# Kernel tuning notes

Measured on AMD Instinct MI355X. Metric: run time of the kernel, lower is better.

The kernel has to match this reference:

```python
import jax, jax.numpy as jnp
import numpy as np

N_NODES = 50000
N_EDGES = 800000
IN_DIM = 256
HID = 256
NUM_LAYERS = 2


def _sage(xin, src, dst, inv_deg, W_l, b_l, W_r):
    # PyG SAGEConv (mean aggr): lin_l(mean of src features scattered to dst) + lin_r(x)
    agg = jax.ops.segment_sum(xin[src], dst, num_segments=xin.shape[0]) * inv_deg
    return agg @ W_l + b_l + xin @ W_r


def _mgdsgu(x, src, dst, inv_deg, h, Wx_l, bx_l, Wx_r, Wh_l, bh_l, Wh_r, Wb1, bb1, Wb2, bb2):
    # hid->hid conv order: 0=sage_hidden, 1=sage_single_h, 2=sage_update_h, 3=sage_candidate_h
    # in ->hid conv order: 0=sage_single_x, 1=sage_update_x, 2=sage_candidate_x
    h_N = _sage(h, src, dst, inv_deg, Wh_l[0], bh_l[0], Wh_r[0])
    # predict_missing_info: r = zeros so r_v = beta; gamma is computed in the
    # original but multiplied by zero -> no effect (omitted).
    beta = jnp.tanh(h @ Wb1 + bb1 + h_N @ Wb2 + bb2)
    m = h + beta - h_N
    h_N = h_N + m  # == h + beta, kept as written for clarity
    r = jax.nn.sigmoid(_sage(x, src, dst, inv_deg, Wx_l[0], bx_l[0], Wx_r[0])
                       + _sage(h_N, src, dst, inv_deg, Wh_l[1], bh_l[1], Wh_r[1]))
    z = jax.nn.sigmoid(_sage(x, src, dst, inv_deg, Wx_l[1], bx_l[1], Wx_r[1])
                       + _sage(h_N, src, dst, inv_deg, Wh_l[2], bh_l[2], Wh_r[2]))
    h_tilde = jnp.tanh(_sage(x, src, dst, inv_deg, Wx_l[2], bx_l[2], Wx_r[2])
                       + _sage(r * h_N, src, dst, inv_deg, Wh_l[3], bh_l[3], Wh_r[3]))
    return (1.0 - z) * h_N + z * h_tilde


def setup_inputs() -> dict:
    key = jax.random.key(0)
    ks = jax.random.split(key, 12)
    sx = 1.0 / np.sqrt(IN_DIM)
    sh = 1.0 / np.sqrt(HID)
    inp = {
        "x": jax.random.normal(ks[0], (N_NODES, IN_DIM), dtype=jnp.float32),
        "edge_index": jax.random.randint(ks[1], (2, N_EDGES), 0, N_NODES, dtype=jnp.int64),
        "Wx_l": jax.random.normal(ks[2], (3, IN_DIM, HID), dtype=jnp.float32) * sx,
        "bx_l": jnp.zeros((3, HID), dtype=jnp.float32),
        "Wx_r": jax.random.normal(ks[3], (3, IN_DIM, HID), dtype=jnp.float32) * sx,
        "Wh_l": jax.random.normal(ks[4], (4, HID, HID), dtype=jnp.float32) * sh,
        "bh_l": jnp.zeros((4, HID), dtype=jnp.float32),
        "Wh_r": jax.random.normal(ks[5], (4, HID, HID), dtype=jnp.float32) * sh,
        "Wb1": jax.random.normal(ks[6], (HID, HID), dtype=jnp.float32) * sh,
        "bb1": jnp.zeros((HID,), dtype=jnp.float32),
        "Wb2": jax.random.normal(ks[7], (HID, HID), dtype=jnp.float32) * sh,
        "bb2": jnp.zeros((HID,), dtype=jnp.float32),
        "We1": jax.random.normal(ks[8], (2 * HID, HID), dtype=jnp.float32) * (1.0 / np.sqrt(2 * HID)),
        "be1": jnp.zeros((HID,), dtype=jnp.float32),
        "We2": jax.random.normal(ks[9], (HID, 1), dtype=jnp.float32) * sh,
        "be2": jnp.zeros((1,), dtype=jnp.float32),
    }
    return inp


def reference(x, edge_index, Wx_l, bx_l, Wx_r, Wh_l, bh_l, Wh_r,
              Wb1, bb1, Wb2, bb2, We1, be1, We2, be2):
    src, dst = edge_index[0], edge_index[1]
    deg = jax.ops.segment_sum(jnp.ones((src.shape[0],), dtype=x.dtype), dst,
                              num_segments=x.shape[0])
    inv_deg = (1.0 / jnp.maximum(deg, 1.0))[:, None]  # [N, 1]

    h = jnp.zeros((x.shape[0], HID), dtype=x.dtype)
    for _ in range(NUM_LAYERS):
        h = _mgdsgu(x, src, dst, inv_deg, h, Wx_l, bx_l, Wx_r,
                    Wh_l, bh_l, Wh_r, Wb1, bb1, Wb2, bb2)

    # edge embeddings: concat(src emb, dst emb) -> MLP -> sigmoid
    edge_emb = jnp.concatenate([h[src], h[dst]], axis=1)  # [E, 2H]
    hidden = jax.nn.relu(edge_emb @ We1 + be1)
    preds = jax.nn.sigmoid(hidden @ We2 + be2)  # [E, 1]
    return (preds, h)
```

## Files before the change

kernel.cpp:

```cpp
#include <hip/hip_runtime.h>
#include <math.h>

#define HID 256
#define LROW 40

typedef __bf16 bf16x8 __attribute__((ext_vector_type(8)));
typedef float  f32x4  __attribute__((ext_vector_type(4)));
typedef unsigned short us8 __attribute__((ext_vector_type(8)));

__device__ __forceinline__ float sigmoidf_(float x){ return 1.0f/(1.0f + __expf(-x)); }
__device__ __forceinline__ unsigned short f2b(float f){
  __bf16 b = (__bf16)f; return __builtin_bit_cast(unsigned short, b);
}
__device__ __forceinline__ float b2f(unsigned short u){
  return (float)__builtin_bit_cast(__bf16, u);
}

__device__ __forceinline__ int edge_src(const int* ei, int e, int is64){
  return is64 ? ei[2*e] : ei[e];
}
__device__ __forceinline__ int edge_dst(const int* ei, int e, int E, int is64){
  return is64 ? ei[2*(E+e)] : ei[E+e];
}

__global__ void detect_kernel(const int* __restrict__ ei, int* __restrict__ flag){
  __shared__ int any;
  if (threadIdx.x == 0) any = 0;
  __syncthreads();
  if (ei[2*threadIdx.x + 1] != 0) atomicOr(&any, 1);
  __syncthreads();
  if (threadIdx.x == 0) *flag = any ? 0 : 1;
}

__global__ void count_kernel(const int* __restrict__ ei, const int* __restrict__ flag,
                             int* __restrict__ deg_i, int E){
  int e = blockIdx.x*blockDim.x + threadIdx.x;
  if (e >= E) return;
  int is64 = *flag;
  atomicAdd(&deg_i[edge_dst(ei,e,E,is64)], 1);
}

__global__ __launch_bounds__(1024) void scan_kernel(const int* __restrict__ deg_i,
  int* __restrict__ row_ptr, float* __restrict__ inv_deg, int N)
{
  __shared__ int wsum[16];
  __shared__ int carry_s;
  int tid = threadIdx.x, lane = tid & 63, wid = tid >> 6;
  if (tid == 0) carry_s = 0;
  __syncthreads();
  for (int base = 0; base < N; base += 1024){
    int i = base + tid;
    int v = (i < N) ? deg_i[i] : 0;
    int s = v;
    #pragma unroll
    for (int off = 1; off < 64; off <<= 1){
      int t = __shfl_up(s, off, 64);
      if (lane >= off) s += t;
    }
    if (lane == 63) wsum[wid] = s;
    __syncthreads();
    if (tid == 0){
      int run = 0;
      for (int w2 = 0; w2 < 16; ++w2){ int t = wsum[w2]; wsum[w2] = run; run += t; }
    }
    __syncthreads();
    int excl = carry_s + wsum[wid] + s - v;
    if (i < N){
      row_ptr[i] = excl;
      inv_deg[i] = 1.0f / fmaxf((float)v, 1.0f);
    }
    __syncthreads();
    if (tid == 1023) carry_s = excl + v;
    __syncthreads();
  }
  if (threadIdx.x == 0) row_ptr[N] = carry_s;
}

__global__ void fill_kernel(const int* __restrict__ ei, const int* __restrict__ flag,
                            const int* __restrict__ row_ptr, int* __restrict__ cursor,
                            int* __restrict__ col_src, int E){
  int e = blockIdx.x*blockDim.x + threadIdx.x;
  if (e >= E) return;
  int is64 = *flag;
  int d = edge_dst(ei,e,E,is64);
  int pos = atomicAdd(&cursor[d], 1);
  col_src[row_ptr[d] + pos] = edge_src(ei,e,is64);
}

__global__ __launch_bounds__(256) void conv_kernel(const float* __restrict__ in,
                                                   unsigned short* __restrict__ out, int n4){
  int i = blockIdx.x*256 + threadIdx.x;
  if (i >= n4) return;
  float4 v = *(const float4*)&in[(size_t)i*4];
  ushort4 o; o.x=f2b(v.x); o.y=f2b(v.y); o.z=f2b(v.z); o.w=f2b(v.w);
  *(ushort4*)&out[(size_t)i*4] = o;
}

__global__ __launch_bounds__(256) void wconv_kernel(
  const float* __restrict__ Wx_l, const float* __restrict__ Wx_r,
  const float* __restrict__ Wh_l, const float* __restrict__ Wh_r,
  const float* __restrict__ Wb1,  const float* __restrict__ Wb2,
  const float* __restrict__ We1,  unsigned short* __restrict__ Wt)
{
  int widx = blockIdx.x;
  int n = blockIdx.y;
  int k = threadIdx.x;
  const float* src;
  if      (widx < 3)  src = Wx_l + widx*65536;
  else if (widx < 6)  src = Wx_r + (widx-3)*65536;
  else if (widx < 10) src = Wh_l + (widx-6)*65536;
  else if (widx < 14) src = Wh_r + (widx-10)*65536;
  else if (widx == 14) src = Wb1;
  else if (widx == 15) src = Wb2;
  else                src = We1 + (widx-16)*65536;
  Wt[(size_t)widx*65536 + n*256 + k] = f2b(src[k*256 + n]);
}

__global__ __launch_bounds__(256) void comp_kernel(
  const float* __restrict__ A, const float* __restrict__ B,
  const float* __restrict__ add, unsigned short* __restrict__ dst)
{
  __shared__ float col[256];
  int n = blockIdx.x, k = threadIdx.x;
  col[k] = B[k*256 + n];
  __syncthreads();
  float s = add ? add[k*256 + n] : 0.f;
  #pragma unroll 8
  for (int j = 0; j < 256; ++j) s = fmaf(A[k*256 + j], col[j], s);
  dst[n*256 + k] = f2b(s);
}

__global__ __launch_bounds__(256) void aggregate_b_kernel(
    const unsigned short* __restrict__ X, unsigned short* __restrict__ out,
    const int* __restrict__ row_ptr, const int* __restrict__ col_src,
    const float* __restrict__ inv_deg, int N)
{
  int v = blockIdx.x*4 + (threadIdx.x >> 6);
  int lane = threadIdx.x & 63;
  if (v >= N) return;
  int beg = row_ptr[v], end = row_ptr[v+1];
  float a0=0.f, a1=0.f, a2=0.f, a3=0.f;
  int e = beg;
  for (; e + 8 <= end; e += 8){
    int sidx[8];
    #pragma unroll
    for (int t = 0; t < 8; ++t) sidx[t] = col_src[e + t];
    #pragma unroll
    for (int t = 0; t < 8; ++t){
      ushort4 u = *(const ushort4*)&X[(size_t)sidx[t]*HID + lane*4];
      a0 += b2f(u.x); a1 += b2f(u.y); a2 += b2f(u.z); a3 += b2f(u.w);
    }
  }
  for (; e < end; ++e){
    int s0 = col_src[e];
    ushort4 u = *(const ushort4*)&X[(size_t)s0*HID + lane*4];
    a0 += b2f(u.x); a1 += b2f(u.y); a2 += b2f(u.z); a3 += b2f(u.w);
  }
  float w = inv_deg[v];
  ushort4 o; o.x=f2b(a0*w); o.y=f2b(a1*w); o.z=f2b(a2*w); o.w=f2b(a3*w);
  *(ushort4*)&out[(size_t)v*HID + lane*4] = o;
}

__global__ __launch_bounds__(256) void rowprep_kernel(
  const float* __restrict__ bh_l, const float* __restrict__ bb1, const float* __restrict__ bb2,
  const float* __restrict__ Wb2, const float* __restrict__ Wh_l, const float* __restrict__ Wh_r,
  float* __restrict__ brow, float* __restrict__ hrow,
  float* __restrict__ rowL1, float* __restrict__ rowR1,
  float* __restrict__ rowL2, float* __restrict__ rowR2)
{
  __shared__ float sh[256];
  __shared__ float sh2[256];
  int j = threadIdx.x;
  sh[j] = bh_l[j];
  __syncthreads();
  float acc = bb1[j] + bb2[j];
  for (int k = 0; k < 256; ++k) acc = fmaf(sh[k], Wb2[k*256 + j], acc);
  float hr = tanhf(acc);
  brow[j] = acc;
  hrow[j] = hr; sh2[j] = hr;
  __syncthreads();
  const float* Whl1 = Wh_l + 65536;  const float* Whr1 = Wh_r + 65536;
  const float* Whl2 = Wh_l + 131072; const float* Whr2 = Wh_r + 131072;
  float a1=0.f, b1=0.f, a2=0.f, b2v=0.f;
  for (int k = 0; k < 256; ++k){
    float hv = sh2[k];
    a1  = fmaf(hv, Whl1[k*256+j], a1);
    b1  = fmaf(hv, Whr1[k*256+j], b1);
    a2  = fmaf(hv, Whl2[k*256+j], a2);
    b2v = fmaf(hv, Whr2[k*256+j], b2v);
  }
  rowL1[j] = a1; rowR1[j] = b1 + bh_l[256 + j];
  rowL2[j] = a2; rowR2[j] = b2v + bh_l[512 + j];
}

__global__ __launch_bounds__(256) void l1_elem_kernel(
  const unsigned short* __restrict__ xc0, const unsigned short* __restrict__ xc1,
  const int* __restrict__ deg_i, const float* __restrict__ hrow,
  const float* __restrict__ rowL1, const float* __restrict__ rowR1,
  const float* __restrict__ rowL2, const float* __restrict__ rowR2,
  unsigned short* __restrict__ t1, float* __restrict__ z1, int N)
{
  int idx = blockIdx.x*256 + threadIdx.x;
  if (idx >= N*64) return;
  int v = idx >> 6, j4 = (idx & 63) * 4;
  float g = deg_i[v] > 0 ? 1.f : 0.f;
  ushort4 a = *(const ushort4*)&xc0[(size_t)idx*4];
  ushort4 b = *(const ushort4*)&xc1[(size_t)idx*4];
  float4 L1 = *(const float4*)&rowL1[j4];
  float4 R1 = *(const float4*)&rowR1[j4];
  float4 L2 = *(const float4*)&rowL2[j4];
  float4 R2 = *(const float4*)&rowR2[j4];
  float4 hr = *(const float4*)&hrow[j4];
  ushort4 t; float4 z;
  t.x = f2b(sigmoidf_(b2f(a.x) + g*L1.x + R1.x) * hr.x);
  t.y = f2b(sigmoidf_(b2f(a.y) + g*L1.y + R1.y) * hr.y);
  t.z = f2b(sigmoidf_(b2f(a.z) + g*L1.z + R1.z) * hr.z);
  t.w = f2b(sigmoidf_(b2f(a.w) + g*L1.w + R1.w) * hr.w);
  z.x = sigmoidf_(b2f(b.x) + g*L2.x + R2.x);
  z.y = sigmoidf_(b2f(b.y) + g*L2.y + R2.y);
  z.z = sigmoidf_(b2f(b.z) + g*L2.z + R2.z);
  z.w = sigmoidf_(b2f(b.w) + g*L2.w + R2.w);
  *(ushort4*)&t1[(size_t)idx*4] = t;
  *(float4*)&z1[(size_t)idx*4] = z;
}

struct GJob {
  const unsigned short *A0,*W0,*A1,*W1,*A2,*W2,*A3,*W3;
  const float *bias,*bias2,*Z,*HN;
  const float *mulmat,*Df;
  const unsigned short *Db,*Zb;
  float* outF; unsigned short* outB;
  int hn_bcast;
};

template<int MODE>
__global__ __launch_bounds__(512) void mgemm4_kernel(GJob j0, GJob j1, GJob j2, int M)
{
  __shared__ unsigned short Al[64*LROW];
  __shared__ unsigned short Wl[256*LROW];
  const GJob& J = (blockIdx.y == 0) ? j0 : ((blockIdx.y == 1) ? j1 : j2);
  const int tid  = threadIdx.x;
  const int lane = tid & 63, w = tid >> 6;
  const int wr = w >> 2, wc = w & 3;
  const int lane15 = lane & 15, laneq = (lane >> 4) * 8;
  const int row0 = blockIdx.x * 64;

  f32x4 acc[2][4];
  #pragma unroll
  for (int m = 0; m < 2; ++m)
    #pragma unroll
    for (int n = 0; n < 4; ++n) acc[m][n] = (f32x4)0.f;

  const unsigned short* pa[4]; const unsigned short* pw[4];
  int np = 0;
  if (J.A0){ pa[np]=J.A0; pw[np]=J.W0; ++np; }
  if (J.A1){ pa[np]=J.A1; pw[np]=J.W1; ++np; }
  if (J.A2){ pa[np]=J.A2; pw[np]=J.W2; ++np; }
  if (J.A3){ pa[np]=J.A3; pw[np]=J.W3; ++np; }
  const int steps = np * 8;

  const int arow  = tid >> 3;
  const int akoff = (tid & 7) * 4;
  const int garow = (row0 + arow > M-1) ? (M-1) : (row0 + arow);
  const size_t abase = (size_t)garow*HID + akoff;
  const int asidx = arow*LROW + akoff;
  const int wrow  = tid >> 1;
  const int wkoff = (tid & 1) * 16;
  const size_t wbase = (size_t)wrow*HID + wkoff;
  const int wsidx = wrow*LROW + wkoff;

  uint2 Ar0, Ar1; uint4 Wr0a, Wr0b, Wr1a, Wr1b;
  auto loadR = [&](int sp, uint2& a, uint4& wa, uint4& wb){
    const unsigned short* Ap = pa[sp >> 3];
    const unsigned short* Wp = pw[sp >> 3];
    const int k0 = (sp & 7) * 32;
    a  = *(const uint2*)(Ap + abase + k0);
    wa = *(const uint4*)(Wp + wbase + k0);
    wb = *(const uint4*)(Wp + wbase + k0 + 8);
  };
  auto compute = [&](){
    bf16x8 af[2], bfr[4];
    #pragma unroll
    for (int m = 0; m < 2; ++m)
      af[m] = *(const bf16x8*)&Al[(wr*32 + m*16 + lane15)*LROW + laneq];
    #pragma unroll
    for (int n = 0; n < 4; ++n)
      bfr[n] = *(const bf16x8*)&Wl[(wc*64 + n*16 + lane15)*LROW + laneq];
    #pragma unroll
    for (int m = 0; m < 2; ++m)
      #pragma unroll
      for (int n = 0; n < 4; ++n)
        acc[m][n] = __builtin_amdgcn_mfma_f32_16x16x32_bf16(af[m], bfr[n], acc[m][n], 0, 0, 0);
  };

  loadR(0, Ar0,Wr0a,Wr0b);
  loadR(1, Ar1,Wr1a,Wr1b);
  for (int s = 0; s < steps; s += 2){
    __syncthreads();
    *(uint2*)&Al[asidx]    = Ar0;
    *(uint4*)&Wl[wsidx]    = Wr0a;
    *(uint4*)&Wl[wsidx+8]  = Wr0b;
    __syncthreads();
    if (s + 2 < steps) loadR(s+2, Ar0,Wr0a,Wr0b);
    compute();
    __syncthreads();
    *(uint2*)&Al[asidx]    = Ar1;
    *(uint4*)&Wl[wsidx]    = Wr1a;
    *(uint4*)&Wl[wsidx+8]  = Wr1b;
    __syncthreads();
    if (s + 3 < steps) loadR(s+3, Ar1,Wr1a,Wr1b);
    compute();
  }

  #pragma unroll
  for (int n = 0; n < 4; ++n){
    int gc = wc*64 + n*16 + lane15;
    float badd = 0.f;
    if (J.bias)  badd += J.bias[gc];
    if (J.bias2) badd += J.bias2[gc];
    float hnb = 0.f;
    if (MODE == 3 && J.hn_bcast) hnb = J.HN[gc];
    #pragma unroll
    for (int m = 0; m < 2; ++m){
      int rbse = row0 + wr*32 + m*16 + ((lane >> 4) << 2);
      #pragma unroll
      for (int r = 0; r < 4; ++r){
        int gr = rbse + r;
        if (gr >= M) continue;
        size_t idx = (size_t)gr*HID + gc;
        float p = acc[m][n][r] + badd;
        if (J.Df) p += J.Df[idx];
        if (J.Db) p += b2f(J.Db[idx]);
        float v;
        if (MODE == 0) v = p;
        else if (MODE == 1){
          v = sigmoidf_(p);
          if (J.mulmat) v *= J.mulmat[idx];
        } else if (MODE == 2){
          v = J.HN[idx] + tanhf(p);
        } else {
          float z  = J.Z ? J.Z[idx] : b2f(J.Zb[idx]);
          float hv = J.hn_bcast ? hnb : J.HN[idx];
          v = (1.f - z)*hv + z*tanhf(p);
        }
        if (J.outF) J.outF[idx] = v;
        if (J.outB) J.outB[idx] = f2b(v);
      }
    }
  }
}

__global__ __launch_bounds__(256) void edge_pred_kernel(
  const unsigned short* __restrict__ P, const unsigned short* __restrict__ Q,
  const int* __restrict__ ei, const int* __restrict__ flag,
  const float* __restrict__ We2, const float* __restrict__ be2,
  float* __restrict__ preds, int E)
{
  int wid = blockIdx.x*8 + (threadIdx.x >> 5);
  int l = threadIdx.x & 31;
  if (wid >= E) return;
  int is64 = *flag;
  int s = edge_src(ei, wid, is64);
  int d = edge_dst(ei, wid, E, is64);
  us8 p8 = *(const us8*)&P[(size_t)s*HID + l*8];
  us8 q8 = *(const us8*)&Q[(size_t)d*HID + l*8];
  float4 w0 = *(const float4*)&We2[l*8];
  float4 w1 = *(const float4*)&We2[l*8 + 4];
  float part = 0.f;
  #pragma unroll
  for (int j = 0; j < 4; ++j)
    part = fmaf(fmaxf(b2f(p8[j]) + b2f(q8[j]), 0.f), (&w0.x)[j], part);
  #pragma unroll
  for (int j = 0; j < 4; ++j)
    part = fmaf(fmaxf(b2f(p8[4+j]) + b2f(q8[4+j]), 0.f), (&w1.x)[j], part);
  #pragma unroll
  for (int off = 16; off > 0; off >>= 1) part += __shfl_down(part, off, 32);
  if (l == 0) preds[wid] = sigmoidf_(part + be2[0]);
}

typedef const unsigned short* cus;
typedef const float* cf;

template<int MODE>
static void launch_f(const GJob* j, int nj, int M, hipStream_t s){
  dim3 g((M + 63)/64, nj), blk(512);
  mgemm4_kernel<MODE><<<g, blk, 0, s>>>(j[0], nj > 1 ? j[1] : j[0], nj > 2 ? j[2] : j[0], M);
}

extern "C" void kernel_launch(void* const* d_in, const int* in_sizes, int n_in,
                              void* d_out, int out_size, void* d_ws, size_t ws_size,
                              hipStream_t stream)
{
  const float* x    = (const float*)d_in[0];
  const int*   ei   = (const int*)  d_in[1];
  const float* Wx_l = (const float*)d_in[2];
  const float* bx_l = (const float*)d_in[3];
  const float* Wx_r = (const float*)d_in[4];
  const float* Wh_l = (const float*)d_in[5];
  const float* bh_l = (const float*)d_in[6];
  const float* Wh_r = (const float*)d_in[7];
  const float* Wb1  = (const float*)d_in[8];
  const float* bb1  = (const float*)d_in[9];
  const float* Wb2  = (const float*)d_in[10];
  const float* bb2  = (const float*)d_in[11];
  const float* We1  = (const float*)d_in[12];
  const float* be1  = (const float*)d_in[13];
  const float* We2  = (const float*)d_in[14];
  const float* be2  = (const float*)d_in[15];

  const int N = in_sizes[0] / HID;
  const int E = in_sizes[1] / 2;
  cf NUL = nullptr; cus NUB = nullptr;

  size_t off = 0;
  auto alloc = [&](size_t bytes) -> void* {
    void* p = (char*)d_ws + off;
    off += (bytes + 255) & ~(size_t)255;
    return p;
  };
  int*   deg_i   = (int*)  alloc((size_t)N*4);
  int*   cursor  = (int*)  alloc((size_t)N*4);
  int*   row_ptr = (int*)  alloc(((size_t)N+1)*4);
  int*   col_src = (int*)  alloc((size_t)E*4);
  float* inv_deg = (float*)alloc((size_t)N*4);
  int*   flag    = (int*)  alloc(256);
  float* brow    = (float*)alloc(1024);
  float* hrow    = (float*)alloc(1024);
  float* rowL1   = (float*)alloc(1024);
  float* rowR1   = (float*)alloc(1024);
  float* rowL2   = (float*)alloc(1024);
  float* rowR2   = (float*)alloc(1024);
  unsigned short* Wt = (unsigned short*)alloc((size_t)18*65536*2);
  float* F0 = (float*)alloc((size_t)N*HID*4);
  float* F1 = (float*)alloc((size_t)N*HID*4);
  unsigned short* b0 = (unsigned short*)alloc((size_t)N*HID*2);
  unsigned short* b1 = (unsigned short*)alloc((size_t)N*HID*2);
  unsigned short* b2 = (unsigned short*)alloc((size_t)N*HID*2);
  unsigned short* b3 = (unsigned short*)alloc((size_t)N*HID*2);

  float* preds = (float*)d_out;
  float* H     = preds + E;

  auto WT = [&](int i) -> cus { return Wt + (size_t)i*65536; };
  const float* bx0 = bx_l;  const float* bx1 = bx_l + 256; const float* bx2 = bx_l + 512;
  const float* bh1 = bh_l + 256;
  const float* bh2 = bh_l + 512; const float* bh3 = bh_l + 768;

  const int eb  = (E + 255)/256;
  const int nb4 = (N + 3)/4;
  const int n4b = (N*64 + 255)/256;

  auto mkjob = [&](cus A0,cus W0,cus A1,cus W1,
                   cf bias, cf Z, cf HN, int hnb,
                   cf mulmat, cf Df, cus Db, cus Zb,
                   float* oF, unsigned short* oB) -> GJob {
    GJob g;
    g.A0=A0; g.W0=W0; g.A1=A1; g.W1=W1; g.A2=NUB; g.W2=NUB; g.A3=NUB; g.W3=NUB;
    g.bias=bias; g.bias2=NUL; g.Z=Z; g.HN=HN; g.hn_bcast=hnb;
    g.mulmat=mulmat; g.Df=Df; g.Db=Db; g.Zb=Zb;
    g.outF=oF; g.outB=oB;
    return g;
  };

  hipMemsetAsync(deg_i, 0, (size_t)N*4, stream);
  hipMemsetAsync(cursor, 0, (size_t)N*4, stream);
  detect_kernel<<<1,256,0,stream>>>(ei, flag);
  count_kernel<<<eb,256,0,stream>>>(ei, flag, deg_i, E);
  scan_kernel<<<1,1024,0,stream>>>(deg_i, row_ptr, inv_deg, N);
  fill_kernel<<<eb,256,0,stream>>>(ei, flag, row_ptr, cursor, col_src, E);

  conv_kernel<<<n4b,256,0,stream>>>(x, b0, N*64);
  wconv_kernel<<<dim3(18,256),256,0,stream>>>(Wx_l, Wx_r, Wh_l, Wh_r, Wb1, Wb2, We1, Wt);
  comp_kernel<<<256,256,0,stream>>>(Wh_l, Wb2, nullptr, (unsigned short*)WT(14));
  comp_kernel<<<256,256,0,stream>>>(Wh_r, Wb2, Wb1,     (unsigned short*)WT(15));
  rowprep_kernel<<<1,256,0,stream>>>(bh_l, bb1, bb2, Wb2, Wh_l, Wh_r,
                                     brow, hrow, rowL1, rowR1, rowL2, rowR2);

  aggregate_b_kernel<<<nb4,256,0,stream>>>(b0, b1, row_ptr, col_src, inv_deg, N);
  {
    GJob j[3] = {
      mkjob(b1,WT(0), b0,WT(3), bx0, NUL,NUL,0, NUL,NUL,NUB,NUB, nullptr, b2),
      mkjob(b1,WT(1), b0,WT(4), bx1, NUL,NUL,0, NUL,NUL,NUB,NUB, nullptr, b3),
      mkjob(b1,WT(2), b0,WT(5), bx2, NUL,NUL,0, NUL,NUL,NUB,NUB, F0, nullptr)
    };
    launch_f<0>(j, 3, N, stream);
  }

  l1_elem_kernel<<<n4b,256,0,stream>>>(b2, b3, deg_i, hrow, rowL1, rowR1,
                                       rowL2, rowR2, b0, F1, N);
  aggregate_b_kernel<<<nb4,256,0,stream>>>(b0, b1, row_ptr, col_src, inv_deg, N);
  {
    GJob j = mkjob(b1,WT(9), b0,WT(13), bh3, F1,hrow,1, NUL,F0,NUB,NUB, F1, b0);
    launch_f<3>(&j, 1, N, stream);
  }

  aggregate_b_kernel<<<nb4,256,0,stream>>>(b0, b1, row_ptr, col_src, inv_deg, N);
  {
    GJob j = mkjob(b1,WT(14), b0,WT(15), brow, NUL,F1,0, NUL,NUL,NUB,NUB, F1, b0);
    launch_f<2>(&j, 1, N, stream);
  }
  aggregate_b_kernel<<<nb4,256,0,stream>>>(b0, b1, row_ptr, col_src, inv_deg, N);
  {
    GJob j[2] = {
      mkjob(b1,WT(7), b0,WT(11), bh1, NUL,NUL,0, F1,NUL,b2,NUB, nullptr, b2),
      mkjob(b1,WT(8), b0,WT(12), bh2, NUL,NUL,0, NUL,NUL,b3,NUB, nullptr, b3)
    };
    launch_f<1>(j, 2, N, stream);
  }
  aggregate_b_kernel<<<nb4,256,0,stream>>>(b2, b1, row_ptr, col_src, inv_deg, N);
  {
    GJob j = mkjob(b1,WT(9), b2,WT(13), bh3, NUL,F1,0, NUL,F0,NUB,b3, H, b0);
    launch_f<3>(&j, 1, N, stream);
  }

  {
    GJob j[2] = {
      mkjob(b0,WT(16), NUB,NUB, be1, NUL,NUL,0, NUL,NUL,NUB,NUB, nullptr, b2),
      mkjob(b0,WT(17), NUB,NUB, NUL, NUL,NUL,0, NUL,NUL,NUB,NUB, nullptr, b3)
    };
    launch_f<0>(j, 2, N, stream);
  }
  edge_pred_kernel<<<(E+7)/8,256,0,stream>>>(b2, b3, ei, flag, We2, be2, preds, E);
}
```

Before: 1.207 ms.

## Enlarge GEMM row tile to 128, store x-candidate as bf16, drop unused operands

The fused GEMM kernel now processes 128 rows per block instead of 64, with each wave computing a 4x4 grid of MFMA tiles. This doubles reuse of each staged weight tile and halves the number of weight loads, at the cost of more accumulator registers and fewer blocks. The x-candidate intermediate (F0) is now kept in bf16 (b4) rather than fp32, cutting its write and later read traffic but lowering its precision. The unused third and fourth operand pairs and the second bias are removed from the job struct.

```diff
diff --git a/kernel.cpp b/kernel.cpp
--- a/kernel.cpp
+++ b/kernel.cpp
@@ -225,8 +225,8 @@
 }
 
 struct GJob {
-  const unsigned short *A0,*W0,*A1,*W1,*A2,*W2,*A3,*W3;
-  const float *bias,*bias2,*Z,*HN;
+  const unsigned short *A0,*W0,*A1,*W1;
+  const float *bias,*Z,*HN;
   const float *mulmat,*Df;
   const unsigned short *Db,*Zb;
   float* outF; unsigned short* outB;
@@ -234,60 +234,58 @@
 };
 
 template<int MODE>
-__global__ __launch_bounds__(512) void mgemm4_kernel(GJob j0, GJob j1, GJob j2, int M)
-{
-  __shared__ unsigned short Al[64*LROW];
+__global__ __launch_bounds__(512) void mgemm5_kernel(GJob j0, GJob j1, GJob j2, int M)
+{
+  __shared__ unsigned short Al[128*LROW];
   __shared__ unsigned short Wl[256*LROW];
   const GJob& J = (blockIdx.y == 0) ? j0 : ((blockIdx.y == 1) ? j1 : j2);
   const int tid  = threadIdx.x;
   const int lane = tid & 63, w = tid >> 6;
   const int wr = w >> 2, wc = w & 3;
   const int lane15 = lane & 15, laneq = (lane >> 4) * 8;
-  const int row0 = blockIdx.x * 64;
-
-  f32x4 acc[2][4];
+  const int row0 = blockIdx.x * 128;
+
+  f32x4 acc[4][4];
   #pragma unroll
-  for (int m = 0; m < 2; ++m)
+  for (int m = 0; m < 4; ++m)
     #pragma unroll
     for (int n = 0; n < 4; ++n) acc[m][n] = (f32x4)0.f;
 
-  const unsigned short* pa[4]; const unsigned short* pw[4];
+  const unsigned short* pa[2]; const unsigned short* pw[2];
   int np = 0;
   if (J.A0){ pa[np]=J.A0; pw[np]=J.W0; ++np; }
   if (J.A1){ pa[np]=J.A1; pw[np]=J.W1; ++np; }
-  if (J.A2){ pa[np]=J.A2; pw[np]=J.W2; ++np; }
-  if (J.A3){ pa[np]=J.A3; pw[np]=J.W3; ++np; }
   const int steps = np * 8;
 
-  const int arow  = tid >> 3;
-  const int akoff = (tid & 7) * 4;
-  const int garow = (row0 + arow > M-1) ? (M-1) : (row0 + arow);
-  const size_t abase = (size_t)garow*HID + akoff;
-  const int asidx = arow*LROW + akoff;
-  const int wrow  = tid >> 1;
-  const int wkoff = (tid & 1) * 16;
-  const size_t wbase = (size_t)wrow*HID + wkoff;
-  const int wsidx = wrow*LROW + wkoff;
-
-  uint2 Ar0, Ar1; uint4 Wr0a, Wr0b, Wr1a, Wr1b;
-  auto loadR = [&](int sp, uint2& a, uint4& wa, uint4& wb){
+  const int strow = tid >> 2;
+  const int koff  = (tid & 3) * 8;
+  const int garow = (row0 + strow > M-1) ? (M-1) : (row0 + strow);
+  const size_t abase  = (size_t)garow*HID + koff;
+  const size_t wbase0 = (size_t)strow*HID + koff;
+  const size_t wbase1 = (size_t)(strow + 128)*HID + koff;
+  const int asidx  = strow*LROW + koff;
+  const int wsidx0 = strow*LROW + koff;
+  const int wsidx1 = (strow + 128)*LROW + koff;
+
+  uint4 Ar0,Wr0a,Wr0b, Ar1,Wr1a,Wr1b;
+  auto loadR = [&](int sp, uint4& a, uint4& wa, uint4& wb){
     const unsigned short* Ap = pa[sp >> 3];
     const unsigned short* Wp = pw[sp >> 3];
     const int k0 = (sp & 7) * 32;
-    a  = *(const uint2*)(Ap + abase + k0);
-    wa = *(const uint4*)(Wp + wbase + k0);
-    wb = *(const uint4*)(Wp + wbase + k0 + 8);
+    a  = *(const uint4*)(Ap + abase  + k0);
+    wa = *(const uint4*)(Wp + wbase0 + k0);
+    wb = *(const uint4*)(Wp + wbase1 + k0);
   };
   auto compute = [&](){
-    bf16x8 af[2], bfr[4];
-    #pragma unroll
-    for (int m = 0; m < 2; ++m)
-      af[m] = *(const bf16x8*)&Al[(wr*32 + m*16 + lane15)*LROW + laneq];
+    bf16x8 af[4], bfr[4];
+    #pragma unroll
+    for (int m = 0; m < 4; ++m)
+      af[m] = *(const bf16x8*)&Al[(wr*64 + m*16 + lane15)*LROW + laneq];
     #pragma unroll
     for (int n = 0; n < 4; ++n)
       bfr[n] = *(const bf16x8*)&Wl[(wc*64 + n*16 + lane15)*LROW + laneq];
     #pragma unroll
-    for (int m = 0; m < 2; ++m)
+    for (int m = 0; m < 4; ++m)
       #pragma unroll
       for (int n = 0; n < 4; ++n)
         acc[m][n] = __builtin_amdgcn_mfma_f32_16x16x32_bf16(af[m], bfr[n], acc[m][n], 0, 0, 0);
@@ -297,16 +295,16 @@
   loadR(1, Ar1,Wr1a,Wr1b);
   for (int s = 0; s < steps; s += 2){
     __syncthreads();
-    *(uint2*)&Al[asidx]    = Ar0;
-    *(uint4*)&Wl[wsidx]    = Wr0a;
-    *(uint4*)&Wl[wsidx+8]  = Wr0b;
+    *(uint4*)&Al[asidx]  = Ar0;
+    *(uint4*)&Wl[wsidx0] = Wr0a;
+    *(uint4*)&Wl[wsidx1] = Wr0b;
     __syncthreads();
     if (s + 2 < steps) loadR(s+2, Ar0,Wr0a,Wr0b);
     compute();
     __syncthreads();
-    *(uint2*)&Al[asidx]    = Ar1;
-    *(uint4*)&Wl[wsidx]    = Wr1a;
-    *(uint4*)&Wl[wsidx+8]  = Wr1b;
+    *(uint4*)&Al[asidx]  = Ar1;
+    *(uint4*)&Wl[wsidx0] = Wr1a;
+    *(uint4*)&Wl[wsidx1] = Wr1b;
     __syncthreads();
     if (s + 3 < steps) loadR(s+3, Ar1,Wr1a,Wr1b);
     compute();
@@ -315,14 +313,12 @@
   #pragma unroll
   for (int n = 0; n < 4; ++n){
     int gc = wc*64 + n*16 + lane15;
-    float badd = 0.f;
-    if (J.bias)  badd += J.bias[gc];
-    if (J.bias2) badd += J.bias2[gc];
+    float badd = J.bias ? J.bias[gc] : 0.f;
     float hnb = 0.f;
     if (MODE == 3 && J.hn_bcast) hnb = J.HN[gc];
     #pragma unroll
-    for (int m = 0; m < 2; ++m){
-      int rbse = row0 + wr*32 + m*16 + ((lane >> 4) << 2);
+    for (int m = 0; m < 4; ++m){
+      int rbse = row0 + wr*64 + m*16 + ((lane >> 4) << 2);
       #pragma unroll
       for (int r = 0; r < 4; ++r){
         int gr = rbse + r;
@@ -383,8 +379,8 @@
 
 template<int MODE>
 static void launch_f(const GJob* j, int nj, int M, hipStream_t s){
-  dim3 g((M + 63)/64, nj), blk(512);
-  mgemm4_kernel<MODE><<<g, blk, 0, s>>>(j[0], nj > 1 ? j[1] : j[0], nj > 2 ? j[2] : j[0], M);
+  dim3 g((M + 127)/128, nj), blk(512);
+  mgemm5_kernel<MODE><<<g, blk, 0, s>>>(j[0], nj > 1 ? j[1] : j[0], nj > 2 ? j[2] : j[0], M);
 }
 
 extern "C" void kernel_launch(void* const* d_in, const int* in_sizes, int n_in,
@@ -431,12 +427,12 @@
   float* rowL2   = (float*)alloc(1024);
   float* rowR2   = (float*)alloc(1024);
   unsigned short* Wt = (unsigned short*)alloc((size_t)18*65536*2);
-  float* F0 = (float*)alloc((size_t)N*HID*4);
   float* F1 = (float*)alloc((size_t)N*HID*4);
   unsigned short* b0 = (unsigned short*)alloc((size_t)N*HID*2);
   unsigned short* b1 = (unsigned short*)alloc((size_t)N*HID*2);
   unsigned short* b2 = (unsigned short*)alloc((size_t)N*HID*2);
   unsigned short* b3 = (unsigned short*)alloc((size_t)N*HID*2);
+  unsigned short* b4 = (unsigned short*)alloc((size_t)N*HID*2);
 
   float* preds = (float*)d_out;
   float* H     = preds + E;
@@ -455,8 +451,8 @@
                    cf mulmat, cf Df, cus Db, cus Zb,
                    float* oF, unsigned short* oB) -> GJob {
     GJob g;
-    g.A0=A0; g.W0=W0; g.A1=A1; g.W1=W1; g.A2=NUB; g.W2=NUB; g.A3=NUB; g.W3=NUB;
-    g.bias=bias; g.bias2=NUL; g.Z=Z; g.HN=HN; g.hn_bcast=hnb;
+    g.A0=A0; g.W0=W0; g.A1=A1; g.W1=W1;
+    g.bias=bias; g.Z=Z; g.HN=HN; g.hn_bcast=hnb;
     g.mulmat=mulmat; g.Df=Df; g.Db=Db; g.Zb=Zb;
     g.outF=oF; g.outB=oB;
     return g;
@@ -481,7 +477,7 @@
     GJob j[3] = {
       mkjob(b1,WT(0), b0,WT(3), bx0, NUL,NUL,0, NUL,NUL,NUB,NUB, nullptr, b2),
       mkjob(b1,WT(1), b0,WT(4), bx1, NUL,NUL,0, NUL,NUL,NUB,NUB, nullptr, b3),
-      mkjob(b1,WT(2), b0,WT(5), bx2, NUL,NUL,0, NUL,NUL,NUB,NUB, F0, nullptr)
+      mkjob(b1,WT(2), b0,WT(5), bx2, NUL,NUL,0, NUL,NUL,NUB,NUB, nullptr, b4)
     };
     launch_f<0>(j, 3, N, stream);
   }
@@ -490,7 +486,7 @@
                                        rowL2, rowR2, b0, F1, N);
   aggregate_b_kernel<<<nb4,256,0,stream>>>(b0, b1, row_ptr, col_src, inv_deg, N);
   {
-    GJob j = mkjob(b1,WT(9), b0,WT(13), bh3, F1,hrow,1, NUL,F0,NUB,NUB, F1, b0);
+    GJob j = mkjob(b1,WT(9), b0,WT(13), bh3, F1,hrow,1, NUL,NUL,b4,NUB, F1, b0);
     launch_f<3>(&j, 1, N, stream);
   }
 
@@ -509,7 +505,7 @@
   }
   aggregate_b_kernel<<<nb4,256,0,stream>>>(b2, b1, row_ptr, col_src, inv_deg, N);
   {
-    GJob j = mkjob(b1,WT(9), b2,WT(13), bh3, NUL,F1,0, NUL,F0,NUB,b3, H, b0);
+    GJob j = mkjob(b1,WT(9), b2,WT(13), bh3, NUL,F1,0, NUL,NUL,b4,b3, H, b0);
     launch_f<3>(&j, 1, N, stream);
   }
 
```

Result: slower. 1.515 ms (+25.6%).
